# Kernel optimization log

Hardware: AMD Instinct MI355X
Metric: run time of the kernel (lower is better)

Reference implementation:

```python
import jax, jax.numpy as jnp
import numpy as np

NUM_HEADS = 12
ROPE_THETA = 10000.0


def _rope_cos_sin(n, hd, dtype):
    inv_freq = 1.0 / (ROPE_THETA ** (np.arange(0, hd, 2, dtype=np.float64) / hd))
    freqs = np.outer(np.arange(n, dtype=np.float64), inv_freq)  # (N, hd/2)
    emb = np.concatenate([freqs, freqs], axis=-1)               # (N, hd)
    return jnp.asarray(np.cos(emb), dtype), jnp.asarray(np.sin(emb), dtype)


def _apply_rope(t, cos, sin):
    # t: (B, H, N, hd); rotate-half convention
    half = t.shape[-1] // 2
    t1, t2 = t[..., :half], t[..., half:]
    rot = jnp.concatenate([-t2, t1], axis=-1)
    return t * cos + rot * sin


def setup_inputs() -> dict:
    key = jax.random.key(0)
    k1, k2, k3 = jax.random.split(key, 3)
    B, N, C = 8, 1024, 768
    x = jax.random.normal(k1, (B, N, C), dtype=jnp.float32)
    w_qkv = jax.random.normal(k2, (C, 3 * C), dtype=jnp.float32) * 0.02
    w_proj = jax.random.normal(k3, (C, C), dtype=jnp.float32) * 0.02
    b_proj = jnp.zeros((C,), dtype=jnp.float32)
    return {"x": x, "w_qkv": w_qkv, "w_proj": w_proj, "b_proj": b_proj}


def reference(x, w_qkv, w_proj, b_proj):
    B, N, C = x.shape
    H = NUM_HEADS
    hd = C // H
    scale = hd ** -0.5
    # qkv: (B,N,3C) -> (B,N,3,H,hd) -> (B,H,3,N,hd)
    qkv = (x @ w_qkv).reshape(B, N, 3, H, hd).transpose(0, 3, 2, 1, 4)
    q, k, v = qkv[:, :, 0], qkv[:, :, 1], qkv[:, :, 2]  # each (B,H,N,hd)
    cos, sin = _rope_cos_sin(N, hd, x.dtype)
    q = _apply_rope(q, cos, sin)
    k = _apply_rope(k, cos, sin)
    attn = jax.nn.softmax(jnp.einsum("bhqd,bhkd->bhqk", q, k) * scale, axis=-1)
    out = jnp.einsum("bhqk,bhkd->bhqd", attn, v)  # (B,H,N,hd)
    out = out.transpose(0, 2, 1, 3).reshape(B, N, C)
    return out @ w_proj + b_proj
```

## Files before the change

### kernel.cpp

```cpp
#include <hip/hip_runtime.h>

typedef unsigned short ushort_t;
typedef __bf16 bf16x8 __attribute__((ext_vector_type(8)));
typedef float f32x4 __attribute__((ext_vector_type(4)));
typedef float f32x16 __attribute__((ext_vector_type(16)));
typedef unsigned short u16x8 __attribute__((ext_vector_type(8)));
typedef unsigned int u32x2 __attribute__((ext_vector_type(2)));
typedef unsigned int u32x4 __attribute__((ext_vector_type(4)));

#define MFMA16(a, b, c) __builtin_amdgcn_mfma_f32_16x16x32_bf16((a), (b), (c), 0, 0, 0)
#define MFMA32(a, b, c) __builtin_amdgcn_mfma_f32_32x32x16_bf16((a), (b), (c), 0, 0, 0)

#define SEQ 1024
#define NHEAD 12
#define HD 64
#define CDIM 768
#define TS 6291456
#define QSCALE 0.1803368801111204f

__device__ __forceinline__ ushort_t f2bf(float f) {
  __bf16 b = (__bf16)f;
  return __builtin_bit_cast(ushort_t, b);
}
__device__ __forceinline__ unsigned pk2(float lo, float hi) {
  return (unsigned)f2bf(lo) | ((unsigned)f2bf(hi) << 16);
}

__device__ __forceinline__ void plswap(unsigned &a, unsigned &b) {
  u32x2 r = __builtin_amdgcn_permlane32_swap(a, b, false, false);
  a = r[0];
  b = r[1];
}

typedef __attribute__((address_space(1))) void gvoid_t;
typedef __attribute__((address_space(3))) void lvoid_t;
__device__ __forceinline__ void async16(const ushort_t* g, ushort_t* l) {
  __builtin_amdgcn_global_load_lds((gvoid_t*)g, (lvoid_t*)l, 16, 0, 0);
}

__device__ __forceinline__ void transpose_body(const float* __restrict__ in,
                                               ushort_t* __restrict__ out,
                                               int R, int C, int bxi, int byi,
                                               float (*tile)[33]) {
  int bx = bxi * 32, by = byi * 32;
  int tx = threadIdx.x & 31, ty = threadIdx.x >> 5;
#pragma unroll
  for (int i = ty; i < 32; i += 8) {
    int r = by + i, c = bx + tx;
    if (r < R && c < C) tile[i][tx] = in[(size_t)r * C + c];
  }
  __syncthreads();
#pragma unroll
  for (int i = ty; i < 32; i += 8) {
    int r = bx + i, c = by + tx;
    if (r < C && c < R) out[(size_t)r * R + c] = f2bf(tile[tx][i]);
  }
}

__global__ void __launch_bounds__(256) prep_all(const float* __restrict__ x,
                                                const float* __restrict__ w_qkv,
                                                const float* __restrict__ w_proj,
                                                ushort_t* __restrict__ xb,
                                                ushort_t* __restrict__ wqkvT,
                                                ushort_t* __restrict__ wprojT,
                                                float* __restrict__ tab) {
  __shared__ float tile[32][33];
  const int bid = blockIdx.x;
  if (bid < 3072) {
    int i = (bid * 256 + threadIdx.x) * 8;
    float4 a = *(const float4*)(x + i);
    float4 b = *(const float4*)(x + i + 4);
    u16x8 r;
    r[0] = f2bf(a.x); r[1] = f2bf(a.y); r[2] = f2bf(a.z); r[3] = f2bf(a.w);
    r[4] = f2bf(b.x); r[5] = f2bf(b.y); r[6] = f2bf(b.z); r[7] = f2bf(b.w);
    *(u16x8*)(xb + i) = r;
  } else if (bid < 3072 + 1728) {
    int t = bid - 3072;
    transpose_body(w_qkv, wqkvT, 768, 2304, t % 72, t / 72, tile);
  } else if (bid < 3072 + 1728 + 576) {
    int t = bid - (3072 + 1728);
    transpose_body(w_proj, wprojT, 768, 768, t % 24, t / 24, tile);
  } else {
    int g = (bid - 5376) * 256 + threadIdx.x;
    int n = g >> 5, j = g & 31;
    double invf = pow(10000.0, -((double)(2 * j)) / 64.0);
    double fr = (double)n * invf;
    tab[g * 2]     = (float)cos(fr);
    tab[g * 2 + 1] = (float)sin(fr);
  }
}

__device__ __forceinline__ void gemm_bt_core(const ushort_t* __restrict__ A,
                                             const ushort_t* __restrict__ Bt,
                                             int K, int bm, int bn,
                                             ushort_t (*ldsA)[4096],
                                             ushort_t (*ldsB)[4096],
                                             f32x4 acc[4][4]) {
  const int tid = threadIdx.x;
  const int lane = tid & 63, wid = tid >> 6;
  const int wm = (wid >> 1) * 64, wn = (wid & 1) * 64;
  const int fr = lane & 15, fq = lane >> 4;
#pragma unroll
  for (int i = 0; i < 4; ++i)
#pragma unroll
    for (int j = 0; j < 4; ++j) acc[i][j] = (f32x4){0.f, 0.f, 0.f, 0.f};

  const int srow = tid >> 2;
  const int scol = (tid & 3) * 8;
  const size_t aOff = (size_t)(bm + srow) * K + scol;
  const size_t bOff = (size_t)(bn + srow) * K + scol;
  const int nIter = K >> 6;

  for (int kt = 0; kt < nIter; ++kt) {
    const int k0 = kt * 64;
#pragma unroll
    for (int h = 0; h < 2; ++h) {
      async16(A + aOff + k0 + h * 32, ldsA[h] + tid * 8);
      async16(A + aOff + (size_t)64 * K + k0 + h * 32, ldsA[h] + 2048 + tid * 8);
      async16(Bt + bOff + k0 + h * 32, ldsB[h] + tid * 8);
      async16(Bt + bOff + (size_t)64 * K + k0 + h * 32, ldsB[h] + 2048 + tid * 8);
    }
    __syncthreads();
#pragma unroll
    for (int ks = 0; ks < 2; ++ks) {
      bf16x8 aF[4], bF[4];
#pragma unroll
      for (int i = 0; i < 4; ++i)
        aF[i] = *(const bf16x8*)(ldsA[ks] + (wm + i * 16 + fr) * 32 + fq * 8);
#pragma unroll
      for (int j = 0; j < 4; ++j)
        bF[j] = *(const bf16x8*)(ldsB[ks] + (wn + j * 16 + fr) * 32 + fq * 8);
#pragma unroll
      for (int i = 0; i < 4; ++i)
#pragma unroll
        for (int j = 0; j < 4; ++j) acc[i][j] = MFMA16(aF[i], bF[j], acc[i][j]);
    }
    __syncthreads();
  }
}

__global__ void __launch_bounds__(256) gemm_qkv(const ushort_t* __restrict__ A,
                                                const ushort_t* __restrict__ Bt,
                                                const float* __restrict__ tab,
                                                ushort_t* __restrict__ qkv) {
  __shared__ __attribute__((aligned(16))) ushort_t ldsA[2][4096];
  __shared__ __attribute__((aligned(16))) ushort_t ldsB[2][4096];
  f32x4 acc[4][4];
  const int f = blockIdx.x;
  const int xcd = f & 7, r = f >> 3;
  const int bm = (xcd * 8 + (r & 7)) * 128;
  const int bn = (r >> 3) * 128;
  gemm_bt_core(A, Bt, CDIM, bm, bn, ldsA, ldsB, acc);
  const int lane = threadIdx.x & 63, wid = threadIdx.x >> 6;
  const int wm = (wid >> 1) * 64, wn = (wid & 1) * 64;
  const int fr = lane & 15, fq = lane >> 4;
  const int tensor = bn / 768;

  if (tensor < 2) {
    ushort_t* dstT = qkv + (size_t)tensor * TS;
    const float qs = (tensor == 0) ? QSCALE : 1.0f;
#pragma unroll
    for (int i = 0; i < 4; ++i) {
#pragma unroll
      for (int jp = 0; jp < 2; ++jp) {
        const int col = bn + wn + jp * 16 + fr;
        const int rem = col - tensor * 768;
        const int h = rem >> 6;
        const int d2 = rem & 31;
#pragma unroll
        for (int rr = 0; rr < 4; ++rr) {
          const int row = bm + wm + i * 16 + fq * 4 + rr;
          const int b = row >> 10, n = row & 1023;
          const float2 cs = ((const float2*)tab)[n * 32 + d2];
          const float av = acc[i][jp][rr], bv = acc[i][jp + 2][rr];
          const float o1 = (av * cs.x - bv * cs.y) * qs;
          const float o2 = (bv * cs.x + av * cs.y) * qs;
          ushort_t* dst = dstT + ((size_t)(b * NHEAD + h) * SEQ + n) * HD + d2;
          dst[0]  = f2bf(o1);
          dst[32] = f2bf(o2);
        }
      }
    }
  } else {
    ushort_t* vt = qkv + 2 * (size_t)TS;
#pragma unroll
    for (int i = 0; i < 4; ++i) {
      const int row0 = bm + wm + i * 16 + fq * 4;
      const int b = row0 >> 10, n0 = row0 & 1023;
#pragma unroll
      for (int j = 0; j < 4; ++j) {
        const int col = bn + wn + j * 16 + fr;
        const int rem = col - 1536;
        const int h = rem >> 6, d = rem & 63;
        u32x2 pk;
        pk[0] = pk2(acc[i][j][0], acc[i][j][1]);
        pk[1] = pk2(acc[i][j][2], acc[i][j][3]);
        *(u32x2*)(vt + ((size_t)(b * NHEAD + h) * HD + d) * SEQ + n0) = pk;
      }
    }
  }
}

__global__ void __launch_bounds__(256) gemm_proj(const ushort_t* __restrict__ A,
                                                 const ushort_t* __restrict__ Bt,
                                                 const float* __restrict__ bias,
                                                 float* __restrict__ Cout) {
  __shared__ __attribute__((aligned(16))) ushort_t ldsA[2][4096];
  __shared__ __attribute__((aligned(16))) ushort_t ldsB[2][4096];
  f32x4 acc[4][4];
  const int f = blockIdx.x;
  const int xcd = f & 7, r = f >> 3;
  const int bm = (xcd * 8 + (r & 7)) * 128;
  const int bn = (r >> 3) * 128;
  gemm_bt_core(A, Bt, CDIM, bm, bn, ldsA, ldsB, acc);
  const int lane = threadIdx.x & 63, wid = threadIdx.x >> 6;
  const int wm = (wid >> 1) * 64, wn = (wid & 1) * 64;
  const int fr = lane & 15, fq = lane >> 4;
#pragma unroll
  for (int i = 0; i < 4; ++i) {
#pragma unroll
    for (int j = 0; j < 4; ++j) {
      const int col = bn + wn + j * 16 + fr;
      const float bv = bias[col];
#pragma unroll
      for (int rr = 0; rr < 4; ++rr) {
        const int row = bm + wm + i * 16 + fq * 4 + rr;
        Cout[(size_t)row * CDIM + col] = acc[i][j][rr] + bv;
      }
    }
  }
}

__global__ void __launch_bounds__(256) attn_fused(const ushort_t* __restrict__ Qb,
                                                  const ushort_t* __restrict__ Kb,
                                                  const ushort_t* __restrict__ VTb,
                                                  ushort_t* __restrict__ Ob) {
  __shared__ __attribute__((aligned(16))) ushort_t ldsK[2][4096];
  __shared__ __attribute__((aligned(16))) ushort_t ldsV[2][4096];

  const int tid = threadIdx.x, lane = tid & 63, wid = tid >> 6;
  const int l31 = lane & 31, h = lane >> 5;

  const int f = blockIdx.x;
  const int xp = f & 7, rest = f >> 3;
  const int g = rest % 12, qb = rest / 12;
  const int head = g * 8 + xp;
  const int q0 = qb * 128;

  const ushort_t* Qh  = Qb  + (size_t)head * (SEQ * HD);
  const ushort_t* Kh  = Kb  + (size_t)head * (SEQ * HD);
  const ushort_t* VTh = VTb + (size_t)head * (HD * SEQ);

  const int qrow = q0 + wid * 32 + l31;
  bf16x8 qF[4];
#pragma unroll
  for (int dk = 0; dk < 4; ++dk)
    qF[dk] = *(const bf16x8*)(Qh + (size_t)qrow * HD + dk * 16 + 8 * h);

  f32x16 ot[2];
#pragma unroll
  for (int dt = 0; dt < 2; ++dt)
#pragma unroll
    for (int i = 0; i < 16; ++i) ot[dt][i] = 0.f;
  float lsum = 0.f;

  const int s0 = tid, s1 = tid + 256;
  const int r0 = s0 >> 3, c0 = ((s0 & 7) - r0) & 7;
  const int r1 = s1 >> 3, c1 = ((s1 & 7) - r1) & 7;

#define ASTAGE(buf, kt)                                                         \
  {                                                                             \
    async16(Kh + (size_t)((kt) * 64 + r0) * HD + c0 * 8, &ldsK[buf][s0 * 8]);   \
    async16(Kh + (size_t)((kt) * 64 + r1) * HD + c1 * 8, &ldsK[buf][s1 * 8]);   \
    async16(VTh + (size_t)r0 * SEQ + (kt) * 64 + c0 * 8, &ldsV[buf][s0 * 8]);   \
    async16(VTh + (size_t)r1 * SEQ + (kt) * 64 + c1 * 8, &ldsV[buf][s1 * 8]);   \
  }

  ASTAGE(0, 0);
  __syncthreads();

  for (int kt = 0; kt < 16; ++kt) {
    const int cur = kt & 1;
    if (kt < 15) ASTAGE(cur ^ 1, kt + 1);

    f32x16 st[2];
    __builtin_amdgcn_s_setprio(1);
#pragma unroll
    for (int ks = 0; ks < 2; ++ks) {
      f32x16 s;
#pragma unroll
      for (int i = 0; i < 16; ++i) s[i] = 0.f;
      const int kr = ks * 32 + l31;
#pragma unroll
      for (int dk = 0; dk < 4; ++dk) {
        const int sw = (dk * 2 + h + kr) & 7;
        bf16x8 kf = *(const bf16x8*)&ldsK[cur][(kr * 8 + sw) * 8];
        s = MFMA32(kf, qF[dk], s);
      }
      st[ks] = s;
    }
    __builtin_amdgcn_s_setprio(0);

    unsigned pk[2][8];
#pragma unroll
    for (int ks = 0; ks < 2; ++ks) {
      float ls = 0.f;
#pragma unroll
      for (int m = 0; m < 8; ++m) {
        const float e0 = __builtin_amdgcn_exp2f(st[ks][2 * m]);
        const float e1 = __builtin_amdgcn_exp2f(st[ks][2 * m + 1]);
        ls += e0 + e1;
        pk[ks][m] = pk2(e0, e1);
      }
      lsum += ls;
    }

#pragma unroll
    for (int kc = 0; kc < 4; ++kc) {
      const int ks = kc >> 1, mb = (kc & 1) * 4;
      unsigned w0 = pk[ks][mb + 0], w2 = pk[ks][mb + 2];
      unsigned w1 = pk[ks][mb + 1], w3 = pk[ks][mb + 3];
      plswap(w0, w2);
      plswap(w1, w3);
      u32x4 bi;
      bi[0] = w0; bi[1] = w1; bi[2] = w2; bi[3] = w3;
      const bf16x8 pf = __builtin_bit_cast(bf16x8, bi);
      __builtin_amdgcn_s_setprio(1);
#pragma unroll
      for (int dt = 0; dt < 2; ++dt) {
        const int dr = dt * 32 + l31;
        const int sw = (kc * 2 + h + dr) & 7;
        bf16x8 vf = *(const bf16x8*)&ldsV[cur][(dr * 8 + sw) * 8];
        ot[dt] = MFMA32(vf, pf, ot[dt]);
      }
      __builtin_amdgcn_s_setprio(0);
    }
    __syncthreads();
  }
#undef ASTAGE

  lsum += __shfl_xor(lsum, 32);
  const float inv = 1.0f / lsum;
  const int b = head / NHEAD, hh = head - b * NHEAD;
  ushort_t* obase = Ob + ((size_t)(b * SEQ + qrow)) * CDIM + hh * HD;
#pragma unroll
  for (int dt = 0; dt < 2; ++dt) {
#pragma unroll
    for (int r2 = 0; r2 < 4; ++r2) {
      const int d = dt * 32 + 8 * r2 + 4 * h;
      u32x2 w;
      w[0] = pk2(ot[dt][4 * r2 + 0] * inv, ot[dt][4 * r2 + 1] * inv);
      w[1] = pk2(ot[dt][4 * r2 + 2] * inv, ot[dt][4 * r2 + 3] * inv);
      *(u32x2*)(obase + d) = w;
    }
  }
}

extern "C" void kernel_launch(void* const* d_in, const int* in_sizes, int n_in,
                              void* d_out, int out_size, void* d_ws, size_t ws_size,
                              hipStream_t stream) {
  const float* x      = (const float*)d_in[0];
  const float* w_qkv  = (const float*)d_in[1];
  const float* w_proj = (const float*)d_in[2];
  const float* b_proj = (const float*)d_in[3];
  float* out = (float*)d_out;
  char* ws = (char*)d_ws;

  ushort_t* xb     = (ushort_t*)(ws + 0);
  ushort_t* wqkvT  = (ushort_t*)(ws + 12582912);
  ushort_t* wprojT = (ushort_t*)(ws + 16121856);
  ushort_t* qkv    = (ushort_t*)(ws + 17301504);
  float*    tab    = (float*)  (ws + 55050240);
  ushort_t* oattn  = (ushort_t*)(ws + 55312384);

  prep_all<<<5504, 256, 0, stream>>>(x, w_qkv, w_proj, xb, wqkvT, wprojT, tab);
  gemm_qkv<<<1152, 256, 0, stream>>>(xb, wqkvT, tab, qkv);
  attn_fused<<<768, 256, 0, stream>>>(qkv, qkv + TS, qkv + 2 * (size_t)TS, oattn);
  gemm_proj<<<384, 256, 0, stream>>>(oattn, wprojT, b_proj, out);
}
```

Before: 197.3 us.

## Triple-buffer GEMM K-loop with async prefetch and swizzled LDS layout

Replaces the load-then-compute GEMM loop in both the QKV and projection GEMMs with a three-stage ring of LDS buffers. Global-to-LDS async copies for later K-steps are issued while MFMAs run on the current one, and progress is gated by vmcnt waits and raw barriers. The LDS chunk layout is also XOR-style rotated by row, which targets bank conflicts on fragment reads. LDS use grows by half, and the hardcoded K=768 with manual waitcnt counts makes the code fragile if shapes or the number of copies per stage change.

```diff
diff --git a/kernel.cpp b/kernel.cpp
--- a/kernel.cpp
+++ b/kernel.cpp
@@ -90,9 +90,29 @@
   }
 }
 
+__device__ __forceinline__ void gemm_compute32(const ushort_t* la, const ushort_t* lb,
+                                               int wm, int wn, int fr, int fq,
+                                               f32x4 acc[4][4]) {
+  bf16x8 aF[4], bF[4];
+#pragma unroll
+  for (int i = 0; i < 4; ++i) {
+    const int R = wm + i * 16 + fr;
+    aF[i] = *(const bf16x8*)(la + R * 32 + (((fq + (R >> 1)) & 3) << 3));
+  }
+#pragma unroll
+  for (int j = 0; j < 4; ++j) {
+    const int S = wn + j * 16 + fr;
+    bF[j] = *(const bf16x8*)(lb + S * 32 + (((fq + (S >> 1)) & 3) << 3));
+  }
+#pragma unroll
+  for (int i = 0; i < 4; ++i)
+#pragma unroll
+    for (int j = 0; j < 4; ++j) acc[i][j] = MFMA16(aF[i], bF[j], acc[i][j]);
+}
+
 __device__ __forceinline__ void gemm_bt_core(const ushort_t* __restrict__ A,
                                              const ushort_t* __restrict__ Bt,
-                                             int K, int bm, int bn,
+                                             int bm, int bn,
                                              ushort_t (*ldsA)[4096],
                                              ushort_t (*ldsB)[4096],
                                              f32x4 acc[4][4]) {
@@ -106,51 +126,65 @@
     for (int j = 0; j < 4; ++j) acc[i][j] = (f32x4){0.f, 0.f, 0.f, 0.f};
 
   const int srow = tid >> 2;
-  const int scol = (tid & 3) * 8;
-  const size_t aOff = (size_t)(bm + srow) * K + scol;
-  const size_t bOff = (size_t)(bn + srow) * K + scol;
-  const int nIter = K >> 6;
-
-  for (int kt = 0; kt < nIter; ++kt) {
-    const int k0 = kt * 64;
-#pragma unroll
-    for (int h = 0; h < 2; ++h) {
-      async16(A + aOff + k0 + h * 32, ldsA[h] + tid * 8);
-      async16(A + aOff + (size_t)64 * K + k0 + h * 32, ldsA[h] + 2048 + tid * 8);
-      async16(Bt + bOff + k0 + h * 32, ldsB[h] + tid * 8);
-      async16(Bt + bOff + (size_t)64 * K + k0 + h * 32, ldsB[h] + 2048 + tid * 8);
-    }
-    __syncthreads();
-#pragma unroll
-    for (int ks = 0; ks < 2; ++ks) {
-      bf16x8 aF[4], bF[4];
-#pragma unroll
-      for (int i = 0; i < 4; ++i)
-        aF[i] = *(const bf16x8*)(ldsA[ks] + (wm + i * 16 + fr) * 32 + fq * 8);
-#pragma unroll
-      for (int j = 0; j < 4; ++j)
-        bF[j] = *(const bf16x8*)(ldsB[ks] + (wn + j * 16 + fr) * 32 + fq * 8);
-#pragma unroll
-      for (int i = 0; i < 4; ++i)
-#pragma unroll
-        for (int j = 0; j < 4; ++j) acc[i][j] = MFMA16(aF[i], bF[j], acc[i][j]);
-    }
-    __syncthreads();
-  }
+  const int scol = (((tid & 3) - (srow >> 1)) & 3) << 3;
+  const ushort_t* aSrc = A + (size_t)(bm + srow) * CDIM + scol;
+  const ushort_t* bSrc = Bt + (size_t)(bn + srow) * CDIM + scol;
+
+#define STAGE_STEP(buf, s)                                                       \
+  {                                                                              \
+    async16(aSrc + (s) * 32, ldsA[buf] + tid * 8);                               \
+    async16(aSrc + (size_t)64 * CDIM + (s) * 32, ldsA[buf] + 2048 + tid * 8);    \
+    async16(bSrc + (s) * 32, ldsB[buf] + tid * 8);                               \
+    async16(bSrc + (size_t)64 * CDIM + (s) * 32, ldsB[buf] + 2048 + tid * 8);    \
+  }
+
+  STAGE_STEP(0, 0);
+  STAGE_STEP(1, 1);
+  STAGE_STEP(2, 2);
+
+#pragma unroll 3
+  for (int s = 0; s < 21; ++s) {
+    const int b = s % 3;
+    asm volatile("s_waitcnt vmcnt(8)" ::: "memory");
+    __builtin_amdgcn_sched_barrier(0);
+    __builtin_amdgcn_s_barrier();
+    __builtin_amdgcn_sched_barrier(0);
+    gemm_compute32(ldsA[b], ldsB[b], wm, wn, fr, fq, acc);
+    __builtin_amdgcn_sched_barrier(0);
+    __builtin_amdgcn_s_barrier();
+    __builtin_amdgcn_sched_barrier(0);
+    STAGE_STEP(b, s + 3);
+  }
+  asm volatile("s_waitcnt vmcnt(8)" ::: "memory");
+  __builtin_amdgcn_sched_barrier(0);
+  __builtin_amdgcn_s_barrier();
+  __builtin_amdgcn_sched_barrier(0);
+  gemm_compute32(ldsA[0], ldsB[0], wm, wn, fr, fq, acc);
+  asm volatile("s_waitcnt vmcnt(4)" ::: "memory");
+  __builtin_amdgcn_sched_barrier(0);
+  __builtin_amdgcn_s_barrier();
+  __builtin_amdgcn_sched_barrier(0);
+  gemm_compute32(ldsA[1], ldsB[1], wm, wn, fr, fq, acc);
+  asm volatile("s_waitcnt vmcnt(0)" ::: "memory");
+  __builtin_amdgcn_sched_barrier(0);
+  __builtin_amdgcn_s_barrier();
+  __builtin_amdgcn_sched_barrier(0);
+  gemm_compute32(ldsA[2], ldsB[2], wm, wn, fr, fq, acc);
+#undef STAGE_STEP
 }
 
 __global__ void __launch_bounds__(256) gemm_qkv(const ushort_t* __restrict__ A,
                                                 const ushort_t* __restrict__ Bt,
                                                 const float* __restrict__ tab,
                                                 ushort_t* __restrict__ qkv) {
-  __shared__ __attribute__((aligned(16))) ushort_t ldsA[2][4096];
-  __shared__ __attribute__((aligned(16))) ushort_t ldsB[2][4096];
+  __shared__ __attribute__((aligned(16))) ushort_t ldsA[3][4096];
+  __shared__ __attribute__((aligned(16))) ushort_t ldsB[3][4096];
   f32x4 acc[4][4];
   const int f = blockIdx.x;
   const int xcd = f & 7, r = f >> 3;
   const int bm = (xcd * 8 + (r & 7)) * 128;
   const int bn = (r >> 3) * 128;
-  gemm_bt_core(A, Bt, CDIM, bm, bn, ldsA, ldsB, acc);
+  gemm_bt_core(A, Bt, bm, bn, ldsA, ldsB, acc);
   const int lane = threadIdx.x & 63, wid = threadIdx.x >> 6;
   const int wm = (wid >> 1) * 64, wn = (wid & 1) * 64;
   const int fr = lane & 15, fq = lane >> 4;
@@ -205,14 +239,14 @@
                                                  const ushort_t* __restrict__ Bt,
                                                  const float* __restrict__ bias,
                                                  float* __restrict__ Cout) {
-  __shared__ __attribute__((aligned(16))) ushort_t ldsA[2][4096];
-  __shared__ __attribute__((aligned(16))) ushort_t ldsB[2][4096];
+  __shared__ __attribute__((aligned(16))) ushort_t ldsA[3][4096];
+  __shared__ __attribute__((aligned(16))) ushort_t ldsB[3][4096];
   f32x4 acc[4][4];
   const int f = blockIdx.x;
   const int xcd = f & 7, r = f >> 3;
   const int bm = (xcd * 8 + (r & 7)) * 128;
   const int bn = (r >> 3) * 128;
-  gemm_bt_core(A, Bt, CDIM, bm, bn, ldsA, ldsB, acc);
+  gemm_bt_core(A, Bt, bm, bn, ldsA, ldsB, acc);
   const int lane = threadIdx.x & 63, wid = threadIdx.x >> 6;
   const int wm = (wid >> 1) * 64, wn = (wid & 1) * 64;
   const int fr = lane & 15, fq = lane >> 4;
```

Result: no change. 196.4 us (-0.4%).
